# Performance work log

Measured on AMD Instinct MI355X. Metric: run time of the kernel, lower is better.

Reference implementation:

```python
import jax, jax.numpy as jnp
import numpy as np

C_IN = 128
C_HID = 32
N_HEADS = 4
INF = 1000000000.0


def setup_inputs() -> dict:
    key = jax.random.key(0)
    ks = jax.random.split(key, 12)
    B, I, J = 1, 256, 256
    hc = N_HEADS * C_HID
    s = 0.02
    return {
        "x": jax.random.normal(ks[0], (B, I, J, C_IN), dtype=jnp.float32),
        "mask": jnp.ones((B, I, J), dtype=jnp.float32),
        "ln_w": jnp.ones((C_IN,), dtype=jnp.float32),
        "ln_b": jnp.zeros((C_IN,), dtype=jnp.float32),
        "w_tri": jax.random.normal(ks[1], (C_IN, N_HEADS), dtype=jnp.float32) * s,
        "wq": jax.random.normal(ks[2], (C_IN, hc), dtype=jnp.float32) * s,
        "wk": jax.random.normal(ks[3], (C_IN, hc), dtype=jnp.float32) * s,
        "wv": jax.random.normal(ks[4], (C_IN, hc), dtype=jnp.float32) * s,
        "wg": jax.random.normal(ks[5], (C_IN, hc), dtype=jnp.float32) * s,
        "bg": jnp.ones((hc,), dtype=jnp.float32),
        "wo": jax.random.normal(ks[6], (hc, C_IN), dtype=jnp.float32) * s,
        "bo": jnp.zeros((C_IN,), dtype=jnp.float32),
    }


def _layer_norm(x, w, b, eps=1e-5):
    mu = jnp.mean(x, axis=-1, keepdims=True)
    var = jnp.var(x, axis=-1, keepdims=True)
    return (x - mu) * jax.lax.rsqrt(var + eps) * w + b


def _triangle_attention(x, mask, ln_w, ln_b, w_tri, wq, wk, wv, wg, bg, wo, bo):
    # starting=True: no transpose. x: [B, I, J, C]
    B, I, J, C = x.shape
    x = _layer_norm(x, ln_w, ln_b)
    # mask_bias: [B, I, 1, 1, J]
    mask_bias = (INF * (mask - 1.0))[..., :, None, None, :]
    # triangle_bias: linear(x) -> [B, I, J, H], permute (2,0,1) -> [B, H, I, J], unsqueeze -> [B, 1, H, I, J]
    tri = jnp.einsum("bijc,ch->bhij", x, w_tri)[:, None]  # [B, 1, H, I, J]
    # q/k/v: [B, I, H, J, Ch]
    def proj(w):
        return jnp.einsum("bijc,c(" + "" + ")->bijc", x, w) if False else (
            (x @ w).reshape(B, I, J, N_HEADS, C_HID).transpose(0, 1, 3, 2, 4))
    q = proj(wq) * (C_HID ** -0.5)
    k = proj(wk)
    v = proj(wv)
    # scores: [B, I, H, J, J]; biases broadcast over H (mask_bias) / I (tri over b,1 dim matches i? no)
    scores = jnp.einsum("bihqc,bihkc->bihqk", q, k)
    scores = scores + mask_bias + tri  # tri [B,1,H,I,J] broadcasts: i-dim aligns with query? matches torch broadcast [B,I,H,J,J]+[B,1,H,J,J]... wait tri is [B,1,H,I,J] with I==J so it broadcasts over the batch-of-rows dim
    a = jax.nn.softmax(scores, axis=-1)
    o = jnp.einsum("bihqk,bihkc->bihqc", a, v)  # [B, I, H, J, Ch]
    o = o.transpose(0, 1, 3, 2, 4).reshape(B, I, J, N_HEADS * C_HID)
    g = jax.nn.sigmoid(x @ wg + bg)
    o = o * g
    return o @ wo + bo  # [B, I, J, C]


def reference(x, mask, ln_w, ln_b, w_tri, wq, wk, wv, wg, bg, wo, bo):
    return _triangle_attention(x, mask, ln_w, ln_b, w_tri, wq, wk, wv, wg, bg, wo, bo)
```

## Files before the change

kernel.cpp:

```cpp
#include <hip/hip_runtime.h>


typedef __attribute__((ext_vector_type(4))) float f32x4;
typedef __attribute__((ext_vector_type(8))) short bf16x8;
#define MFMA16(a, b, c) __builtin_amdgcn_mfma_f32_16x16x32_bf16(a, b, c, 0, 0, 0)
#define LOG2E 1.4426950408889634f

__device__ __forceinline__ float bf2f(unsigned int u16) {
    return __uint_as_float(u16 << 16);
}
__device__ __forceinline__ unsigned int f2bf(float f) {
    unsigned int u = __float_as_uint(f);
    return (u + 0x7fffu + ((u >> 16) & 1u)) >> 16;
}
__device__ __forceinline__ unsigned int pack2(float a, float b) {
    return f2bf(a) | (f2bf(b) << 16);
}
__device__ __forceinline__ unsigned int cvt_pk_bf16(float lo, float hi) {
    unsigned int r;
    asm("v_cvt_pk_bf16_f32 %0, %1, %2" : "=v"(r) : "v"(lo), "v"(hi));
    return r;
}
__device__ __forceinline__ void barrier_lgkm() {
    asm volatile("s_waitcnt lgkmcnt(0)" ::: "memory");
    __builtin_amdgcn_s_barrier();
}

__global__ __launch_bounds__(128) void k_prep(
    const float* __restrict__ wq, const float* __restrict__ wk,
    const float* __restrict__ wv, const float* __restrict__ wg,
    const float* __restrict__ wo, unsigned short* __restrict__ wT)
{
    const int mat = blockIdx.x, k0 = blockIdx.y * 16, t = threadIdx.x;
    const float* W = (mat == 0) ? wq : (mat == 1) ? wk : (mat == 2) ? wv
                     : (mat == 3) ? wg : wo;
    unsigned short* T = wT + mat * 16384;
    float col[16];
    #pragma unroll
    for (int kk = 0; kk < 16; ++kk) col[kk] = W[(k0 + kk) * 128 + t];
    unsigned int pk[8];
    #pragma unroll
    for (int u = 0; u < 8; ++u) pk[u] = pack2(col[2 * u], col[2 * u + 1]);
    *(uint4*)(T + t * 128 + k0)     = make_uint4(pk[0], pk[1], pk[2], pk[3]);
    *(uint4*)(T + t * 128 + k0 + 8) = make_uint4(pk[4], pk[5], pk[6], pk[7]);
}

__global__ __launch_bounds__(256, 2) void k_lnproj(
    const float* __restrict__ x, const float* __restrict__ ln_w,
    const float* __restrict__ ln_b, const float* __restrict__ w_tri,
    const unsigned short* __restrict__ wT, const float* __restrict__ bg,
    unsigned short* __restrict__ qb, unsigned short* __restrict__ kb,
    unsigned short* __restrict__ vtb, unsigned short* __restrict__ gb,
    unsigned short* __restrict__ triTb)
{
    __shared__ unsigned short sA[128 * 136];
    __shared__ unsigned short sB[128 * 136];
    __shared__ unsigned short sWt[16 * 136];

    const int t = threadIdx.x, w = t >> 6, lane = t & 63;
    const int l15 = lane & 15, g = lane >> 4;
    const int rowBase = blockIdx.x * 128;
    const int r2 = t >> 1, half2 = t & 1;

    if (t < 128) {
        const float4 wv = ((const float4*)w_tri)[t];
        sWt[0 * 136 + t] = (unsigned short)f2bf(wv.x);
        sWt[1 * 136 + t] = (unsigned short)f2bf(wv.y);
        sWt[2 * 136 + t] = (unsigned short)f2bf(wv.z);
        sWt[3 * 136 + t] = (unsigned short)f2bf(wv.w);
    } else {
        #pragma unroll
        for (int u = 0; u < 13; ++u) {
            const int idx = (t - 128) + 128 * u;
            if (idx < 12 * 136) sWt[4 * 136 + idx] = 0;
        }
    }

    {
        const float* xr = x + (size_t)(rowBase + r2) * 128 + half2 * 64;
        float v[64];
        float s1 = 0.0f, s2 = 0.0f;
        #pragma unroll
        for (int u = 0; u < 16; ++u) {
            const float4 q4 = ((const float4*)xr)[u];
            v[4*u] = q4.x; v[4*u+1] = q4.y; v[4*u+2] = q4.z; v[4*u+3] = q4.w;
            s1 += q4.x + q4.y + q4.z + q4.w;
            s2 += q4.x*q4.x + q4.y*q4.y + q4.z*q4.z + q4.w*q4.w;
        }
        s1 += __shfl_xor(s1, 1);
        s2 += __shfl_xor(s2, 1);
        const float mu = s1 * (1.0f / 128.0f);
        const float rs = rsqrtf(s2 * (1.0f / 128.0f) - mu * mu + 1e-5f);
        const float4* lw = (const float4*)(ln_w + half2 * 64);
        const float4* lb = (const float4*)(ln_b + half2 * 64);
        #pragma unroll
        for (int u = 0; u < 16; ++u) {
            const float4 w4 = lw[u], b4 = lb[u];
            v[4*u]   = (v[4*u]   - mu) * rs * w4.x + b4.x;
            v[4*u+1] = (v[4*u+1] - mu) * rs * w4.y + b4.y;
            v[4*u+2] = (v[4*u+2] - mu) * rs * w4.z + b4.z;
            v[4*u+3] = (v[4*u+3] - mu) * rs * w4.w + b4.w;
        }
        #pragma unroll
        for (int u = 0; u < 8; ++u) {
            uint4 pk;
            pk.x = pack2(v[8*u],   v[8*u+1]);
            pk.y = pack2(v[8*u+2], v[8*u+3]);
            pk.z = pack2(v[8*u+4], v[8*u+5]);
            pk.w = pack2(v[8*u+6], v[8*u+7]);
            *(uint4*)&sA[r2 * 136 + half2 * 64 + u * 8] = pk;
        }
    }

    {
        const unsigned short* Wm = wT + r2 * 128 + half2 * 64;
        #pragma unroll
        for (int u = 0; u < 8; ++u)
            *(uint4*)&sB[r2 * 136 + half2 * 64 + u * 8] = *(const uint4*)(Wm + u * 8);
    }
    __syncthreads();

    bf16x8 af[2][4];
    #pragma unroll
    for (int m = 0; m < 2; ++m)
        #pragma unroll
        for (int ks = 0; ks < 4; ++ks)
            af[m][ks] = *(const bf16x8*)&sA[(w * 32 + m * 16 + l15) * 136 + ks * 32 + g * 8];

    #pragma unroll
    for (int m = 0; m < 2; ++m) {
        f32x4 tc = (f32x4){0.f, 0.f, 0.f, 0.f};
        #pragma unroll
        for (int ks = 0; ks < 4; ++ks) {
            const bf16x8 bfw = *(const bf16x8*)&sWt[l15 * 136 + ks * 32 + g * 8];
            tc = MFMA16(af[m][ks], bfw, tc);
        }
        if (l15 < 4) {
            #pragma unroll
            for (int reg = 0; reg < 4; ++reg) {
                const int gr = rowBase + w * 32 + m * 16 + 4 * g + reg;
                triTb[l15 * 65536 + gr] = (unsigned short)f2bf(tc[reg] * LOG2E);
            }
        }
    }

    for (int mat = 0; mat < 4; ++mat) {
        f32x4 acc[2][8];
        #pragma unroll
        for (int m = 0; m < 2; ++m)
            #pragma unroll
            for (int n = 0; n < 8; ++n) acc[m][n] = (f32x4){0.f, 0.f, 0.f, 0.f};
        #pragma unroll
        for (int n = 0; n < 8; ++n)
            #pragma unroll
            for (int ks = 0; ks < 4; ++ks) {
                const bf16x8 bf = *(const bf16x8*)&sB[(n * 16 + l15) * 136 + ks * 32 + g * 8];
                acc[0][n] = MFMA16(af[0][ks], bf, acc[0][n]);
                acc[1][n] = MFMA16(af[1][ks], bf, acc[1][n]);
            }
        barrier_lgkm();

        float bgv[8];
        if (mat == 3) {
            #pragma unroll
            for (int n = 0; n < 8; ++n) bgv[n] = bg[n * 16 + l15];
        }
        const float scl = (mat == 0) ? 0.25503486245f : 1.0f;
        #pragma unroll
        for (int m = 0; m < 2; ++m)
            #pragma unroll
            for (int n = 0; n < 8; ++n) {
                float vv[4];
                #pragma unroll
                for (int reg = 0; reg < 4; ++reg) {
                    float z = acc[m][n][reg];
                    if (mat == 3) z = 1.0f / (1.0f + __expf(-(z + bgv[n])));
                    else z *= scl;
                    vv[reg] = z;
                }
                const unsigned int a01 = cvt_pk_bf16(vv[0], vv[1]);
                const unsigned int a23 = cvt_pk_bf16(vv[2], vv[3]);
                const int qr = w * 32 + m * 16 + g * 4;
                const int col = n * 16 + l15;
                sA[qr * 136 + col]       = (unsigned short)a01;
                sA[(qr + 1) * 136 + col] = (unsigned short)(a01 >> 16);
                sA[(qr + 2) * 136 + col] = (unsigned short)a23;
                sA[(qr + 3) * 136 + col] = (unsigned short)(a23 >> 16);
            }
        barrier_lgkm();

        if (mat < 3) {
            const unsigned short* Wm = wT + (mat + 1) * 16384 + r2 * 128 + half2 * 64;
            #pragma unroll
            for (int u = 0; u < 8; ++u)
                *(uint4*)&sB[r2 * 136 + half2 * 64 + u * 8] = *(const uint4*)(Wm + u * 8);
        }

        const int row = rowBase + r2;
        if (mat < 2) {
            unsigned short* dst = (mat == 0) ? qb : kb;
            const int i = row >> 8, j = row & 255;
            #pragma unroll
            for (int u = 0; u < 8; ++u) {
                const int c0 = half2 * 64 + u * 8;
                const int hh = c0 >> 5, ch = c0 & 31;
                *(uint4*)(dst + (((size_t)(i * 4 + hh)) * 256 + j) * 32 + ch) =
                    *(const uint4*)&sA[r2 * 136 + c0];
            }
        } else if (mat == 2) {
            const int c = t & 127, jh = t >> 7;
            const int i = rowBase >> 8;
            const int j0 = (rowBase & 255) + jh * 64;
            unsigned short buf[64];
            #pragma unroll
            for (int u = 0; u < 64; ++u) buf[u] = sA[(jh * 64 + u) * 136 + c];
            unsigned short* dst = vtb + ((size_t)(i * 128 + c)) * 256 + j0;
            #pragma unroll
            for (int u = 0; u < 8; ++u)
                *(uint4*)(dst + u * 8) = *(uint4*)&buf[u * 8];
        } else {
            #pragma unroll
            for (int u = 0; u < 8; ++u) {
                const int c0 = half2 * 64 + u * 8;
                *(uint4*)(gb + (size_t)row * 128 + c0) = *(const uint4*)&sA[r2 * 136 + c0];
            }
        }
        barrier_lgkm();
    }
}

__global__ __launch_bounds__(256, 3) void k_attn6d(
    const unsigned short* __restrict__ qb, const unsigned short* __restrict__ kb,
    const unsigned short* __restrict__ vtb, const float* __restrict__ mask,
    const unsigned short* __restrict__ triTb, const unsigned short* __restrict__ gb,
    unsigned short* __restrict__ ob)
{
    __shared__ unsigned short sK[256 * 32];
    __shared__ unsigned short sVt[32 * 260];
    __shared__ unsigned short sP[4][64 * 36];
    __shared__ float sM[256];

    const int i = blockIdx.x, h = blockIdx.y, t = threadIdx.x;
    const int w = t >> 6, lane = t & 63, l15 = lane & 15, g = lane >> 4;
    const size_t base = (size_t)(i * 4 + h) * 8192;

    {
        const uint4* ks = (const uint4*)(kb + base + t * 32);
        char* kdst = (char*)sK + t * 64;
        const int kswz = (t & 3) << 4;
        #pragma unroll
        for (int u = 0; u < 4; ++u)
            *(uint4*)(kdst + ((u * 16) ^ kswz)) = ks[u];

        const int ch = t >> 3, seg = t & 7;
        const uint4* vs = (const uint4*)(vtb + base + (size_t)ch * 256 + seg * 32);
        unsigned short* vdst = &sVt[ch * 260 + seg * 32];
        #pragma unroll
        for (int u = 0; u < 4; ++u)
            *(uint4*)(vdst + u * 8) = vs[u];

        sM[t] = (LOG2E * 1.0e9f) * (mask[i * 256 + t] - 1.0f);
    }

    const int q0 = w * 64;
    bf16x8 qf[4];
    #pragma unroll
    for (int m = 0; m < 4; ++m)
        qf[m] = *(const bf16x8*)(qb + base + (size_t)(q0 + m * 16 + l15) * 32 + g * 8);

    bf16x8 ones;
    #pragma unroll
    for (int u = 0; u < 8; ++u) ones[u] = (short)0x3F80;

    const unsigned short* triQ = triTb + h * 65536;
    ushort4 tbuf[2][4][2];
    #pragma unroll
    for (int m = 0; m < 4; ++m)
        #pragma unroll
        for (int n2 = 0; n2 < 2; ++n2)
            tbuf[0][m][n2] = *(const ushort4*)
                (triQ + (q0 + m * 16 + l15) * 256 + n2 * 16 + g * 4);

    __syncthreads();

    f32x4 acc[4][2], accL[4];
    #pragma unroll
    for (int m = 0; m < 4; ++m) {
        acc[m][0] = (f32x4){0.f, 0.f, 0.f, 0.f};
        acc[m][1] = (f32x4){0.f, 0.f, 0.f, 0.f};
        accL[m]   = (f32x4){0.f, 0.f, 0.f, 0.f};
    }

    unsigned short* sPw = &sP[w][0];

    #pragma unroll
    for (int kt = 0; kt < 4; ++kt) {
        const int kv0 = kt * 64;
        #pragma unroll
        for (int hh = 0; hh < 2; ++hh) {
            const int kvh = kv0 + hh * 32;
            const int s = kt * 2 + hh;
            const int ph = s & 1;

            if (s < 7) {
                const int nkvh = ((s + 1) >> 1) * 64 + ((s + 1) & 1) * 32;
                #pragma unroll
                for (int m = 0; m < 4; ++m)
                    #pragma unroll
                    for (int n2 = 0; n2 < 2; ++n2)
                        tbuf[ph ^ 1][m][n2] = *(const ushort4*)
                            (triQ + (q0 + m * 16 + l15) * 256 + nkvh + n2 * 16 + g * 4);
            }

            bf16x8 kf[2];
            #pragma unroll
            for (int n2 = 0; n2 < 2; ++n2) {
                const int row = kvh + n2 * 16 + l15;
                kf[n2] = *(const bf16x8*)((const char*)sK + row * 64 +
                                          ((g * 16) ^ ((row & 3) << 4)));
            }
            float4 mk[2];
            #pragma unroll
            for (int n2 = 0; n2 < 2; ++n2)
                mk[n2] = *(const float4*)&sM[kvh + n2 * 16 + g * 4];

            #pragma unroll
            for (int m = 0; m < 4; ++m) {
                f32x4 p[2];
                #pragma unroll
                for (int n2 = 0; n2 < 2; ++n2) {
                    const ushort4 tv = tbuf[ph][m][n2];
                    f32x4 cb;
                    cb[0] = mk[n2].x + bf2f(tv.x);
                    cb[1] = mk[n2].y + bf2f(tv.y);
                    cb[2] = mk[n2].z + bf2f(tv.z);
                    cb[3] = mk[n2].w + bf2f(tv.w);
                    p[n2] = MFMA16(kf[n2], qf[m], cb);
                }
                #pragma unroll
                for (int n2 = 0; n2 < 2; ++n2) {
                    p[n2][0] = exp2f(p[n2][0]);
                    p[n2][1] = exp2f(p[n2][1]);
                    p[n2][2] = exp2f(p[n2][2]);
                    p[n2][3] = exp2f(p[n2][3]);
                }
                #pragma unroll
                for (int n2 = 0; n2 < 2; ++n2) {
                    const unsigned int a01 = cvt_pk_bf16(p[n2][0], p[n2][1]);
                    const unsigned int a23 = cvt_pk_bf16(p[n2][2], p[n2][3]);
                    *(uint2*)&sPw[(m * 16 + l15) * 36 + n2 * 16 + g * 4] =
                        make_uint2(a01, a23);
                }
            }

            const bf16x8 vf0 = *(const bf16x8*)&sVt[l15 * 260 + kvh + g * 8];
            const bf16x8 vf1 = *(const bf16x8*)&sVt[(16 + l15) * 260 + kvh + g * 8];
            #pragma unroll
            for (int m = 0; m < 4; ++m) {
                const bf16x8 pb = *(const bf16x8*)&sPw[(m * 16 + l15) * 36 + g * 8];
                acc[m][0] = MFMA16(vf0, pb, acc[m][0]);
                acc[m][1] = MFMA16(vf1, pb, acc[m][1]);
                accL[m]   = MFMA16(ones, pb, accL[m]);
            }
        }
    }

    #pragma unroll
    for (int m = 0; m < 4; ++m) {
        const float inv = 1.0f / accL[m][0];
        const int q = q0 + m * 16 + l15;
        const unsigned short* gp = gb + (size_t)(i * 256 + q) * 128 + h * 32;
        unsigned short* op = ob + (((size_t)(i * 256 + q)) * 4 + h) * 32;
        #pragma unroll
        for (int n2 = 0; n2 < 2; ++n2) {
            const uint2 gv = *(const uint2*)(gp + n2 * 16 + g * 4);
            const float g0 = bf2f(gv.x & 0xffffu), g1 = bf2f(gv.x >> 16);
            const float g2 = bf2f(gv.y & 0xffffu), g3 = bf2f(gv.y >> 16);
            const unsigned int a01 =
                cvt_pk_bf16(acc[m][n2][0] * inv * g0, acc[m][n2][1] * inv * g1);
            const unsigned int a23 =
                cvt_pk_bf16(acc[m][n2][2] * inv * g2, acc[m][n2][3] * inv * g3);
            *(uint2*)(op + n2 * 16 + g * 4) = make_uint2(a01, a23);
        }
    }
}

__global__ __launch_bounds__(256, 3) void k_out3(
    const unsigned short* __restrict__ ob, const unsigned short* __restrict__ woT,
    const float* __restrict__ bo, float* __restrict__ out)
{
    __shared__ unsigned short sA[128 * 136];
    __shared__ unsigned short sB[128 * 72];
    const int t = threadIdx.x, w = t >> 6, lane = t & 63;
    const int l15 = lane & 15, g = lane >> 4;
    const int rowBase = blockIdx.x * 128;
    const int r = t >> 1, half = t & 1;

    #pragma unroll
    for (int u = 0; u < 8; ++u) {
        const int c = half * 64 + u * 8;
        *(uint4*)&sA[r * 136 + c] = *(const uint4*)(ob + (size_t)(rowBase + r) * 128 + c);
    }

    f32x4 acc[2][8];
    #pragma unroll
    for (int m = 0; m < 2; ++m)
        #pragma unroll
        for (int n = 0; n < 8; ++n) acc[m][n] = (f32x4){0.f, 0.f, 0.f, 0.f};

    #pragma unroll
    for (int kc = 0; kc < 2; ++kc) {
        #pragma unroll
        for (int u = 0; u < 4; ++u)
            *(uint4*)&sB[r * 72 + half * 32 + u * 8] =
                *(const uint4*)(woT + r * 128 + kc * 64 + half * 32 + u * 8);
        __syncthreads();
        #pragma unroll
        for (int ks = 0; ks < 2; ++ks) {
            const bf16x8 a0 = *(const bf16x8*)
                &sA[(w * 32 + l15) * 136 + kc * 64 + ks * 32 + g * 8];
            const bf16x8 a1 = *(const bf16x8*)
                &sA[(w * 32 + 16 + l15) * 136 + kc * 64 + ks * 32 + g * 8];
            #pragma unroll
            for (int n = 0; n < 8; ++n) {
                const bf16x8 bf = *(const bf16x8*)&sB[(n * 16 + l15) * 72 + ks * 32 + g * 8];
                acc[0][n] = MFMA16(a0, bf, acc[0][n]);
                acc[1][n] = MFMA16(a1, bf, acc[1][n]);
            }
        }
        __syncthreads();
    }

    float bov[8];
    #pragma unroll
    for (int n = 0; n < 8; ++n) bov[n] = bo[n * 16 + l15];
    #pragma unroll
    for (int m = 0; m < 2; ++m)
        #pragma unroll
        for (int n = 0; n < 8; ++n)
            #pragma unroll
            for (int reg = 0; reg < 4; ++reg) {
                const int row = rowBase + w * 32 + m * 16 + g * 4 + reg;
                out[(size_t)row * 128 + n * 16 + l15] = acc[m][n][reg] + bov[n];
            }
}

extern "C" void kernel_launch(void* const* d_in, const int* in_sizes, int n_in,
                              void* d_out, int out_size, void* d_ws, size_t ws_size,
                              hipStream_t stream) {
    (void)in_sizes; (void)n_in; (void)out_size; (void)ws_size;
    const float* x     = (const float*)d_in[0];
    const float* mask  = (const float*)d_in[1];
    const float* ln_w  = (const float*)d_in[2];
    const float* ln_b  = (const float*)d_in[3];
    const float* w_tri = (const float*)d_in[4];
    const float* wq    = (const float*)d_in[5];
    const float* wk    = (const float*)d_in[6];
    const float* wv    = (const float*)d_in[7];
    const float* wg    = (const float*)d_in[8];
    const float* bg    = (const float*)d_in[9];
    const float* wo    = (const float*)d_in[10];
    const float* bo    = (const float*)d_in[11];
    float* out = (float*)d_out;

    char* ws = (char*)d_ws;
    unsigned short* qb    = (unsigned short*)(ws + (16u << 20));
    unsigned short* kb    = (unsigned short*)(ws + (32u << 20));
    unsigned short* vtb   = (unsigned short*)(ws + (48u << 20));
    unsigned short* gb    = (unsigned short*)(ws + (64u << 20));
    unsigned short* ob    = (unsigned short*)(ws + (80u << 20));
    unsigned short* triTb = (unsigned short*)(ws + (96u << 20));
    unsigned short* wT    = (unsigned short*)(ws + (97u << 20));

    k_prep<<<dim3(5, 8), 128, 0, stream>>>(wq, wk, wv, wg, wo, wT);
    k_lnproj<<<512, 256, 0, stream>>>(x, ln_w, ln_b, w_tri, wT, bg,
                                      qb, kb, vtb, gb, triTb);
    k_attn6d<<<dim3(256, 4), 256, 0, stream>>>(qb, kb, vtb, mask, triTb, gb, ob);
    k_out3<<<512, 256, 0, stream>>>(ob, wT + 4 * 16384, bo, out);
}
```

Baseline: 100.6 us.

## Halve weight LDS buffer in k_lnproj via K-split staging and register prefetch

The projection kernel now stages each weight matrix into shared memory in two K-halves, holding the next half in registers while the current half is consumed. The triangle-bias weights are pre-converted to bf16 in k_prep and read straight from global memory, which removes their shared buffer. Shared memory per block drops so the launch bound can go from 2 to 3 blocks per CU. The cost is extra barriers per matrix, more registers for the prefetch, and uncached-looking global reads for the triangle weights.

```diff
diff --git a/kernel.cpp b/kernel.cpp
--- a/kernel.cpp
+++ b/kernel.cpp
@@ -29,9 +29,23 @@
 __global__ __launch_bounds__(128) void k_prep(
     const float* __restrict__ wq, const float* __restrict__ wk,
     const float* __restrict__ wv, const float* __restrict__ wg,
-    const float* __restrict__ wo, unsigned short* __restrict__ wT)
+    const float* __restrict__ wo, const float* __restrict__ w_tri,
+    unsigned short* __restrict__ wT, unsigned short* __restrict__ wtT)
 {
-    const int mat = blockIdx.x, k0 = blockIdx.y * 16, t = threadIdx.x;
+    const int mat = blockIdx.x, t = threadIdx.x;
+    if (mat == 5) {
+        if (blockIdx.y == 0) {
+            const float4 wv4 = ((const float4*)w_tri)[t];
+            wtT[0 * 128 + t] = (unsigned short)f2bf(wv4.x);
+            wtT[1 * 128 + t] = (unsigned short)f2bf(wv4.y);
+            wtT[2 * 128 + t] = (unsigned short)f2bf(wv4.z);
+            wtT[3 * 128 + t] = (unsigned short)f2bf(wv4.w);
+            #pragma unroll
+            for (int n = 4; n < 16; ++n) wtT[n * 128 + t] = 0;
+        }
+        return;
+    }
+    const int k0 = blockIdx.y * 16;
     const float* W = (mat == 0) ? wq : (mat == 1) ? wk : (mat == 2) ? wv
                      : (mat == 3) ? wg : wo;
     unsigned short* T = wT + mat * 16384;
@@ -45,36 +59,21 @@
     *(uint4*)(T + t * 128 + k0 + 8) = make_uint4(pk[4], pk[5], pk[6], pk[7]);
 }
 
-__global__ __launch_bounds__(256, 2) void k_lnproj(
+__global__ __launch_bounds__(256, 3) void k_lnproj(
     const float* __restrict__ x, const float* __restrict__ ln_w,
-    const float* __restrict__ ln_b, const float* __restrict__ w_tri,
+    const float* __restrict__ ln_b, const unsigned short* __restrict__ wtT,
     const unsigned short* __restrict__ wT, const float* __restrict__ bg,
     unsigned short* __restrict__ qb, unsigned short* __restrict__ kb,
     unsigned short* __restrict__ vtb, unsigned short* __restrict__ gb,
     unsigned short* __restrict__ triTb)
 {
     __shared__ unsigned short sA[128 * 136];
-    __shared__ unsigned short sB[128 * 136];
-    __shared__ unsigned short sWt[16 * 136];
+    __shared__ unsigned short sB[128 * 72];
 
     const int t = threadIdx.x, w = t >> 6, lane = t & 63;
     const int l15 = lane & 15, g = lane >> 4;
     const int rowBase = blockIdx.x * 128;
     const int r2 = t >> 1, half2 = t & 1;
-
-    if (t < 128) {
-        const float4 wv = ((const float4*)w_tri)[t];
-        sWt[0 * 136 + t] = (unsigned short)f2bf(wv.x);
-        sWt[1 * 136 + t] = (unsigned short)f2bf(wv.y);
-        sWt[2 * 136 + t] = (unsigned short)f2bf(wv.z);
-        sWt[3 * 136 + t] = (unsigned short)f2bf(wv.w);
-    } else {
-        #pragma unroll
-        for (int u = 0; u < 13; ++u) {
-            const int idx = (t - 128) + 128 * u;
-            if (idx < 12 * 136) sWt[4 * 136 + idx] = 0;
-        }
-    }
 
     {
         const float* xr = x + (size_t)(rowBase + r2) * 128 + half2 * 64;
@@ -113,10 +112,16 @@
     }
 
     {
-        const unsigned short* Wm = wT + r2 * 128 + half2 * 64;
-        #pragma unroll
-        for (int u = 0; u < 8; ++u)
-            *(uint4*)&sB[r2 * 136 + half2 * 64 + u * 8] = *(const uint4*)(Wm + u * 8);
+        const unsigned short* Wm = wT + r2 * 128 + half2 * 32;
+        #pragma unroll
+        for (int u = 0; u < 4; ++u)
+            *(uint4*)&sB[r2 * 72 + half2 * 32 + u * 8] = *(const uint4*)(Wm + u * 8);
+    }
+    uint4 wreg[4];
+    {
+        const unsigned short* p = wT + r2 * 128 + 64 + half2 * 32;
+        #pragma unroll
+        for (int u = 0; u < 4; ++u) wreg[u] = *(const uint4*)(p + u * 8);
     }
     __syncthreads();
 
@@ -132,7 +137,7 @@
         f32x4 tc = (f32x4){0.f, 0.f, 0.f, 0.f};
         #pragma unroll
         for (int ks = 0; ks < 4; ++ks) {
-            const bf16x8 bfw = *(const bf16x8*)&sWt[l15 * 136 + ks * 32 + g * 8];
+            const bf16x8 bfw = *(const bf16x8*)(wtT + l15 * 128 + ks * 32 + g * 8);
             tc = MFMA16(af[m][ks], bfw, tc);
         }
         if (l15 < 4) {
@@ -150,15 +155,45 @@
         for (int m = 0; m < 2; ++m)
             #pragma unroll
             for (int n = 0; n < 8; ++n) acc[m][n] = (f32x4){0.f, 0.f, 0.f, 0.f};
+
         #pragma unroll
         for (int n = 0; n < 8; ++n)
             #pragma unroll
-            for (int ks = 0; ks < 4; ++ks) {
-                const bf16x8 bf = *(const bf16x8*)&sB[(n * 16 + l15) * 136 + ks * 32 + g * 8];
+            for (int ks = 0; ks < 2; ++ks) {
+                const bf16x8 bf = *(const bf16x8*)&sB[(n * 16 + l15) * 72 + ks * 32 + g * 8];
                 acc[0][n] = MFMA16(af[0][ks], bf, acc[0][n]);
                 acc[1][n] = MFMA16(af[1][ks], bf, acc[1][n]);
             }
         barrier_lgkm();
+
+        #pragma unroll
+        for (int u = 0; u < 4; ++u)
+            *(uint4*)&sB[r2 * 72 + half2 * 32 + u * 8] = wreg[u];
+        if (mat < 3) {
+            const unsigned short* p = wT + (mat + 1) * 16384 + r2 * 128 + half2 * 32;
+            #pragma unroll
+            for (int u = 0; u < 4; ++u) wreg[u] = *(const uint4*)(p + u * 8);
+        }
+        barrier_lgkm();
+
+        #pragma unroll
+        for (int n = 0; n < 8; ++n)
+            #pragma unroll
+            for (int ks = 0; ks < 2; ++ks) {
+                const bf16x8 bf = *(const bf16x8*)&sB[(n * 16 + l15) * 72 + ks * 32 + g * 8];
+                acc[0][n] = MFMA16(af[0][2 + ks], bf, acc[0][n]);
+                acc[1][n] = MFMA16(af[1][2 + ks], bf, acc[1][n]);
+            }
+        barrier_lgkm();
+
+        if (mat < 3) {
+            #pragma unroll
+            for (int u = 0; u < 4; ++u)
+                *(uint4*)&sB[r2 * 72 + half2 * 32 + u * 8] = wreg[u];
+            const unsigned short* p = wT + (mat + 1) * 16384 + r2 * 128 + 64 + half2 * 32;
+            #pragma unroll
+            for (int u = 0; u < 4; ++u) wreg[u] = *(const uint4*)(p + u * 8);
+        }
 
         float bgv[8];
         if (mat == 3) {
@@ -188,13 +223,6 @@
                 sA[(qr + 3) * 136 + col] = (unsigned short)(a23 >> 16);
             }
         barrier_lgkm();
-
-        if (mat < 3) {
-            const unsigned short* Wm = wT + (mat + 1) * 16384 + r2 * 128 + half2 * 64;
-            #pragma unroll
-            for (int u = 0; u < 8; ++u)
-                *(uint4*)&sB[r2 * 136 + half2 * 64 + u * 8] = *(const uint4*)(Wm + u * 8);
-        }
 
         const int row = rowBase + r2;
         if (mat < 2) {
@@ -471,9 +499,10 @@
     unsigned short* ob    = (unsigned short*)(ws + (80u << 20));
     unsigned short* triTb = (unsigned short*)(ws + (96u << 20));
     unsigned short* wT    = (unsigned short*)(ws + (97u << 20));
-
-    k_prep<<<dim3(5, 8), 128, 0, stream>>>(wq, wk, wv, wg, wo, wT);
-    k_lnproj<<<512, 256, 0, stream>>>(x, ln_w, ln_b, w_tri, wT, bg,
+    unsigned short* wtT   = (unsigned short*)(ws + (97u << 20) + 163840);
+
+    k_prep<<<dim3(6, 8), 128, 0, stream>>>(wq, wk, wv, wg, wo, w_tri, wT, wtT);
+    k_lnproj<<<512, 256, 0, stream>>>(x, ln_w, ln_b, wtT, wT, bg,
                                       qb, kb, vtb, gb, triTb);
     k_attn6d<<<dim3(256, 4), 256, 0, stream>>>(qb, kb, vtb, mask, triTb, gb, ob);
     k_out3<<<512, 256, 0, stream>>>(ob, wT + 4 * 16384, bo, out);
```

Result: slower. 116.4 us (+15.7%).
